# Kernel tuning notes

Measured on AMD Instinct MI355X. Metric: run time of the kernel, lower is better.

Reference implementation:

```python
import jax, jax.numpy as jnp
import numpy as np

N_NODES = 100000

def _gcn_conv(x, W, b, src, dst, ew, num_nodes):
    # x: [N, Fin], W: [Fin, Fout], src/dst: [Etot], ew: [Etot]
    xw = x @ W                                   # [N, Fout]
    deg = jax.ops.segment_sum(ew, dst, num_segments=num_nodes)   # [N]
    dinv = jnp.where(deg > 0, jax.lax.rsqrt(jnp.where(deg > 0, deg, 1.0)), 0.0)
    norm = dinv[src] * ew * dinv[dst]            # [Etot]
    msg = xw[src] * norm[:, None]                # [Etot, Fout] gather-transform
    out = jax.ops.segment_sum(msg, dst, num_segments=num_nodes)  # scatter-add
    return out + b

def setup_inputs() -> dict:
    key = jax.random.key(0)
    k1, k2, k3, k4, k5, k6, k7 = jax.random.split(key, 7)
    N, E, F_IN, HID, CLS = N_NODES, 1600000, 128, 64, 32
    x = jax.random.normal(k1, (N, F_IN), dtype=jnp.float32)
    edge_index = jax.random.randint(k2, (2, E), 0, N, dtype=jnp.int64)
    edge_weight = jax.random.uniform(k3, (E,), dtype=jnp.float32)
    s1 = 1.0 / np.sqrt(F_IN)
    s2 = 1.0 / np.sqrt(HID)
    W1 = jax.random.uniform(k4, (F_IN, HID), dtype=jnp.float32, minval=-s1, maxval=s1)
    b1 = jnp.zeros((HID,), dtype=jnp.float32)
    W2 = jax.random.uniform(k5, (HID, CLS), dtype=jnp.float32, minval=-s2, maxval=s2)
    b2 = jnp.zeros((CLS,), dtype=jnp.float32)
    return {"x": x, "edge_index": edge_index, "edge_weight": edge_weight,
            "W1": W1, "b1": b1, "W2": W2, "b2": b2}

def reference(x, edge_index, edge_weight, W1, b1, W2, b2):
    N = x.shape[0]
    # add self-loops with weight 1 (PyG GCNConv default)
    loop = jnp.arange(N, dtype=edge_index.dtype)
    src = jnp.concatenate([edge_index[0], loop])
    dst = jnp.concatenate([edge_index[1], loop])
    ew = jnp.concatenate([edge_weight, jnp.ones((N,), dtype=edge_weight.dtype)])
    h = _gcn_conv(x, W1, b1, src, dst, ew, N)
    h = jax.nn.relu(h)
    # dropout is identity in eval mode
    out = _gcn_conv(h, W2, b2, src, dst, ew, N)
    return out
```

## Files before the change

### kernel.cpp

```cpp
#include <hip/hip_runtime.h>

#define FIN 128
#define HID 64
#define CLS 32

#define BSH 7
#define BNODES 128
#define GB 256
#define BCAP 4096
#define SCAP 6272
#define NBUKP 800

using bfrag = __attribute__((ext_vector_type(8))) short;
using cfrag = __attribute__((ext_vector_type(4))) float;

__device__ inline unsigned short f2bf(float x) {
  unsigned u = __float_as_uint(x);
  return (unsigned short)((u + 0x7FFFu + ((u >> 16) & 1u)) >> 16);
}
__device__ inline void bf8_to_f32(int4 v, float* f) {
  f[0] = __uint_as_float((unsigned)v.x << 16);
  f[1] = __uint_as_float((unsigned)v.x & 0xFFFF0000u);
  f[2] = __uint_as_float((unsigned)v.y << 16);
  f[3] = __uint_as_float((unsigned)v.y & 0xFFFF0000u);
  f[4] = __uint_as_float((unsigned)v.z << 16);
  f[5] = __uint_as_float((unsigned)v.z & 0xFFFF0000u);
  f[6] = __uint_as_float((unsigned)v.w << 16);
  f[7] = __uint_as_float((unsigned)v.w & 0xFFFF0000u);
}

__global__ __launch_bounds__(1024) void k_sort_wpack(const int* __restrict__ src,
                                                     const int* __restrict__ dst,
                                                     const float* __restrict__ ew,
                                                     int2* __restrict__ recsA,
                                                     int* __restrict__ gcntT,
                                                     int* __restrict__ loffB,
                                                     const float* __restrict__ W1,
                                                     const float* __restrict__ W2,
                                                     unsigned short* __restrict__ wp1,
                                                     unsigned short* __restrict__ wp2,
                                                     int E, int CHUNK, int NBUK) {
  __shared__ int2 stage[SCAP];
  __shared__ int lcnt[NBUKP];
  __shared__ int loff[NBUKP];
  __shared__ int lcur[NBUKP];
  __shared__ int ssum[1024];
  const int b = blockIdx.x, t = threadIdx.x;

  if (b >= GB) {
    int t2 = (b - GB) * 1024 + t;
    for (int i = t2; i < 16 * 512; i += 2048) {
      int f = i >> 9, l = (i >> 3) & 63, j = i & 7;
      int ks = f >> 2, nt = f & 3;
      int k = ks * 32 + (l >> 4) * 8 + j;
      int n = nt * 16 + (l & 15);
      wp1[i] = f2bf(W1[k * 64 + n]);
    }
    for (int i = t2; i < 4 * 512; i += 2048) {
      int f = i >> 9, l = (i >> 3) & 63, j = i & 7;
      int ks = f >> 1, nt = f & 1;
      int k = ks * 32 + (l >> 4) * 8 + j;
      int n = nt * 16 + (l & 15);
      wp2[i] = f2bf(W2[k * 32 + n]);
    }
    return;
  }

  const int s = b * CHUNK, e = min(E, s + CHUNK);
  const int m = e - s;

  for (int i = t; i < NBUK; i += 1024) lcnt[i] = 0;
  __syncthreads();
  for (int p = s + t; p < e; p += 1024)
    atomicAdd(&lcnt[dst[p] >> BSH], 1);
  __syncthreads();

  int c = (t < NBUK) ? lcnt[t] : 0;
  ssum[t] = c;
  __syncthreads();
  for (int off = 1; off < 1024; off <<= 1) {
    int v = (t >= off) ? ssum[t - off] : 0;
    __syncthreads();
    ssum[t] += v;
    __syncthreads();
  }
  if (t < NBUK) { loff[t] = ssum[t] - c; lcur[t] = ssum[t] - c; }
  if (t == 0) loff[NBUK] = m;
  __syncthreads();

  for (int p = s + t; p < e; p += 1024) {
    int d = dst[p];
    int bk = d >> BSH;
    int pos = atomicAdd(&lcur[bk], 1);
    stage[pos] = make_int2(src[p] | ((d & (BNODES - 1)) << 17), __float_as_int(ew[p]));
  }
  __syncthreads();

  for (int p = t; p < m; p += 1024) recsA[s + p] = stage[p];
  for (int i = t; i < NBUK; i += 1024) gcntT[i * GB + b] = lcnt[i];
  for (int i = t; i <= NBUK; i += 1024) loffB[b * NBUKP + i] = loff[i];
}

__global__ __launch_bounds__(256) void k_scan_sums(const int* __restrict__ counts,
                                                   int* __restrict__ bsum, int N) {
  __shared__ int s[256];
  int base = blockIdx.x * 4096 + threadIdx.x * 16;
  int t = 0;
#pragma unroll
  for (int j = 0; j < 16; ++j)
    if (base + j < N) t += counts[base + j];
  s[threadIdx.x] = t;
  __syncthreads();
  for (int off = 128; off > 0; off >>= 1) {
    if (threadIdx.x < off) s[threadIdx.x] += s[threadIdx.x + off];
    __syncthreads();
  }
  if (threadIdx.x == 0) bsum[blockIdx.x] = s[0];
}

__global__ __launch_bounds__(256) void k_scan_emit(const int* __restrict__ counts,
                                                   const int* __restrict__ bsum,
                                                   int* __restrict__ rowstart, int N, int nb) {
  __shared__ int sb[256];
  __shared__ int s[256];
  const int t = threadIdx.x;
  int bv = (t < nb) ? bsum[t] : 0;
  sb[t] = bv;
  __syncthreads();
  for (int off = 1; off < 256; off <<= 1) {
    int u = (t >= off) ? sb[t - off] : 0;
    __syncthreads();
    sb[t] += u;
    __syncthreads();
  }
  sb[t] -= bv;
  __syncthreads();
  const int bbase = sb[blockIdx.x];

  int base = blockIdx.x * 4096 + t * 16;
  int c[16];
  int tsum = 0;
#pragma unroll
  for (int j = 0; j < 16; ++j) {
    c[j] = (base + j < N) ? counts[base + j] : 0;
    tsum += c[j];
  }
  s[t] = tsum;
  __syncthreads();
  for (int off = 1; off < 256; off <<= 1) {
    int v = (t >= off) ? s[t - off] : 0;
    __syncthreads();
    s[t] += v;
    __syncthreads();
  }
  int run = bbase + s[t] - tsum;
#pragma unroll
  for (int j = 0; j < 16; ++j) {
    if (base + j < N) rowstart[base + j] = run;
    run += c[j];
  }
}

__global__ __launch_bounds__(256) void k_bucket(const int2* __restrict__ recsA,
                                                const int* __restrict__ goff,
                                                const int* __restrict__ loffB,
                                                int2* __restrict__ pairs,
                                                float* __restrict__ dinv,
                                                int* __restrict__ rowstart,
                                                int N, int E, int CHUNK, int NBUK) {
  __shared__ int2 lrec[BCAP];
  __shared__ int2 sout[BCAP];
  __shared__ int cnt[BNODES];
  __shared__ int cur[BNODES];
  __shared__ int sbuf[BNODES];
  __shared__ float degs[BNODES];
  __shared__ float dl[BNODES];
  const int b = blockIdx.x;
  const int t = threadIdx.x;
  const int bstart = goff[b * GB];
  const int bend = (b + 1 < NBUK) ? goff[(b + 1) * GB] : E;
  int m = bend - bstart;
  if (m > BCAP) m = BCAP;

  if (t < BNODES) { cnt[t] = 0; degs[t] = 1.0f; }
  __syncthreads();

  {
    int ls = loffB[t * NBUKP + b];
    int le = loffB[t * NBUKP + b + 1];
    int doff = goff[b * GB + t] - bstart;
    const int2* sp = recsA + (size_t)t * CHUNK + ls;
    int len = le - ls;
    for (int j = 0; j < len; ++j) {
      if (doff + j < BCAP) lrec[doff + j] = sp[j];
    }
  }
  __syncthreads();

  for (int p = t; p < m; p += 256) {
    int2 r = lrec[p];
    int d = (r.x >> 17) & (BNODES - 1);
    atomicAdd(&cnt[d], 1);
    atomicAdd(&degs[d], __int_as_float(r.y));
  }
  __syncthreads();
  if (t < BNODES) sbuf[t] = cnt[t];
  __syncthreads();
  for (int off = 1; off < BNODES; off <<= 1) {
    int v = (t < BNODES && t >= off) ? sbuf[t - off] : 0;
    __syncthreads();
    if (t < BNODES) sbuf[t] += v;
    __syncthreads();
  }
  if (t < BNODES) {
    int ls = sbuf[t] - cnt[t];
    cur[t] = ls;
    float di = rsqrtf(degs[t]);
    dl[t] = di;
    int node = b * BNODES + t;
    if (node < N) { dinv[node] = di; rowstart[node] = bstart + ls; }
  }
  __syncthreads();
  for (int p = t; p < m; p += 256) {
    int2 r = lrec[p];
    int d = (r.x >> 17) & (BNODES - 1);
    int pos = atomicAdd(&cur[d], 1);
    float c = __int_as_float(r.y) * dl[d];
    sout[pos] = make_int2(r.x & 0x1FFFF, __float_as_int(c));
  }
  __syncthreads();
  for (int p = t; p < m; p += 256) pairs[bstart + p] = sout[p];
}

template <int K, int F, bool ABF16>
__global__ __launch_bounds__(256, 4) void mfma_gemm(const void* __restrict__ xv,
                                                    const unsigned short* __restrict__ wp,
                                                    const float* __restrict__ scale,
                                                    unsigned short* __restrict__ y, int N) {
  constexpr int KS = K / 32;
  constexpr int NT = F / 16;
  const int lane = threadIdx.x & 63;
  const int quad = lane >> 4;
  const int col = lane & 15;
  const int row0 = blockIdx.x * 64 + (threadIdx.x >> 6) * 16;
  if (row0 >= N) return;

  bfrag bf[KS * NT];
#pragma unroll
  for (int f = 0; f < KS * NT; ++f)
    bf[f] = *(const bfrag*)(wp + f * 512 + lane * 8);

  cfrag acc[NT] = {};

  int row_a = row0 + col;
  if (row_a >= N) row_a = N - 1;

#pragma unroll
  for (int ks = 0; ks < KS; ++ks) {
    bfrag af;
    if (ABF16) {
      const unsigned short* xp = (const unsigned short*)xv + (size_t)row_a * K + quad * 8;
      af = *(const bfrag*)(xp + ks * 32);
    } else {
      const float* xp = (const float*)xv + (size_t)row_a * K + quad * 8;
      float4 a0 = *(const float4*)(xp + ks * 32);
      float4 a1 = *(const float4*)(xp + ks * 32 + 4);
      af[0] = (short)f2bf(a0.x); af[1] = (short)f2bf(a0.y);
      af[2] = (short)f2bf(a0.z); af[3] = (short)f2bf(a0.w);
      af[4] = (short)f2bf(a1.x); af[5] = (short)f2bf(a1.y);
      af[6] = (short)f2bf(a1.z); af[7] = (short)f2bf(a1.w);
    }
#pragma unroll
    for (int nt = 0; nt < NT; ++nt)
      acc[nt] = __builtin_amdgcn_mfma_f32_16x16x32_bf16(af, bf[ks * NT + nt], acc[nt], 0, 0, 0);
  }

  float scr[4];
#pragma unroll
  for (int r = 0; r < 4; ++r) {
    int row = row0 + quad * 4 + r;
    scr[r] = (row < N) ? scale[row] : 0.f;
  }
#pragma unroll
  for (int nt = 0; nt < NT; ++nt)
#pragma unroll
    for (int r = 0; r < 4; ++r) {
      int row = row0 + quad * 4 + r;
      if (row < N)
        y[(size_t)row * F + nt * 16 + col] = f2bf(scr[r] * acc[nt][r]);
    }
}

template <int F, bool BF16OUT>
__global__ __launch_bounds__(256) void pull_agg(const unsigned short* __restrict__ xs,
                                                const int2* __restrict__ pairs,
                                                const int* __restrict__ rowstart,
                                                const float* __restrict__ dinv,
                                                const float* __restrict__ b,
                                                void* __restrict__ outv, int N, int E) {
  constexpr int LPN = F / 8;
  constexpr int NPB = 256 / LPN;
  const int g = blockIdx.x * NPB + threadIdx.x / LPN;
  const int f8 = (threadIdx.x % LPN) * 8;
  if (g >= N) return;

  const int start = rowstart[g];
  const int end = (g + 1 < N) ? rowstart[g + 1] : E;
  const float di = dinv[g];

  float acc[8];
  {
    int4 v = *(const int4*)&xs[(size_t)g * F + f8];
    float xf[8];
    bf8_to_f32(v, xf);
    float4 b0 = *(const float4*)&b[f8];
    float4 b1 = *(const float4*)&b[f8 + 4];
    acc[0] = fmaf(di, xf[0], b0.x); acc[1] = fmaf(di, xf[1], b0.y);
    acc[2] = fmaf(di, xf[2], b0.z); acc[3] = fmaf(di, xf[3], b0.w);
    acc[4] = fmaf(di, xf[4], b1.x); acc[5] = fmaf(di, xf[5], b1.y);
    acc[6] = fmaf(di, xf[6], b1.z); acc[7] = fmaf(di, xf[7], b1.w);
  }

  int p = start;
  for (; p + 2 <= end; p += 2) {
    int2 p0 = pairs[p];
    int2 p1 = pairs[p + 1];
    int4 v0 = *(const int4*)&xs[(size_t)p0.x * F + f8];
    int4 v1 = *(const int4*)&xs[(size_t)p1.x * F + f8];
    float c0 = __int_as_float(p0.y), c1 = __int_as_float(p1.y);
    float x0[8], x1[8];
    bf8_to_f32(v0, x0);
    bf8_to_f32(v1, x1);
#pragma unroll
    for (int j = 0; j < 8; ++j) acc[j] = fmaf(c0, x0[j], acc[j]);
#pragma unroll
    for (int j = 0; j < 8; ++j) acc[j] = fmaf(c1, x1[j], acc[j]);
  }
  if (p < end) {
    int2 pa = pairs[p];
    int4 va = *(const int4*)&xs[(size_t)pa.x * F + f8];
    float ca = __int_as_float(pa.y);
    float xa[8];
    bf8_to_f32(va, xa);
#pragma unroll
    for (int j = 0; j < 8; ++j) acc[j] = fmaf(ca, xa[j], acc[j]);
  }

  if (BF16OUT) {
    unsigned short* out = (unsigned short*)outv;
    ushort4 o0, o1;
    o0.x = f2bf(fmaxf(acc[0], 0.f)); o0.y = f2bf(fmaxf(acc[1], 0.f));
    o0.z = f2bf(fmaxf(acc[2], 0.f)); o0.w = f2bf(fmaxf(acc[3], 0.f));
    o1.x = f2bf(fmaxf(acc[4], 0.f)); o1.y = f2bf(fmaxf(acc[5], 0.f));
    o1.z = f2bf(fmaxf(acc[6], 0.f)); o1.w = f2bf(fmaxf(acc[7], 0.f));
    *(ushort4*)&out[(size_t)g * F + f8] = o0;
    *(ushort4*)&out[(size_t)g * F + f8 + 4] = o1;
  } else {
    float* out = (float*)outv;
    *(float4*)&out[(size_t)g * F + f8] = make_float4(acc[0], acc[1], acc[2], acc[3]);
    *(float4*)&out[(size_t)g * F + f8 + 4] = make_float4(acc[4], acc[5], acc[6], acc[7]);
  }
}

extern "C" void kernel_launch(void* const* d_in, const int* in_sizes, int n_in,
                              void* d_out, int out_size, void* d_ws, size_t ws_size,
                              hipStream_t stream) {
  const float* x  = (const float*)d_in[0];
  const int*   ei = (const int*)d_in[1];
  const float* ew = (const float*)d_in[2];
  const float* W1 = (const float*)d_in[3];
  const float* b1 = (const float*)d_in[4];
  const float* W2 = (const float*)d_in[5];
  const float* b2 = (const float*)d_in[6];
  float* out = (float*)d_out;

  const int N = in_sizes[0] / FIN;
  const int E = in_sizes[2];
  const int* src = ei;
  const int* dst = ei + E;

  const int NBUK = (N + BNODES - 1) >> BSH;
  const int M = NBUK * GB;
  const int CHUNK = (E + GB - 1) / GB;
  const int nbM = (M + 4095) / 4096;

  float* wsf      = (float*)d_ws;
  float* dinv     = wsf;
  int*   rowstart = (int*)(dinv + N);
  int*   gcntT    = rowstart + N;
  int*   loffB    = gcntT + M;
  int*   bsum     = loffB + GB * NBUKP;
  int2*  recsA    = (int2*)(bsum + 256);
  int2*  pairs    = recsA + E;
  unsigned short* xs1 = (unsigned short*)(pairs + E);
  unsigned short* out1b = xs1 + (size_t)N * HID;
  unsigned short* xs2 = xs1;
  unsigned short* wp1 = out1b + (size_t)N * HID;
  unsigned short* wp2 = wp1 + 16 * 512;

  k_sort_wpack<<<GB + 2, 1024, 0, stream>>>(src, dst, ew, recsA, gcntT, loffB,
                                            W1, W2, wp1, wp2, E, CHUNK, NBUK);
  k_scan_sums<<<nbM, 256, 0, stream>>>(gcntT, bsum, M);
  k_scan_emit<<<nbM, 256, 0, stream>>>(gcntT, bsum, gcntT, M, nbM);
  k_bucket<<<NBUK, 256, 0, stream>>>(recsA, gcntT, loffB, pairs, dinv, rowstart,
                                     N, E, CHUNK, NBUK);

  mfma_gemm<FIN, HID, false><<<(N + 63) / 64, 256, 0, stream>>>(x, wp1, dinv, xs1, N);
  pull_agg<HID, true><<<(N + 31) / 32, 256, 0, stream>>>(xs1, pairs, rowstart, dinv, b1, out1b, N, E);

  mfma_gemm<HID, CLS, true><<<(N + 63) / 64, 256, 0, stream>>>(out1b, wp2, dinv, xs2, N);
  pull_agg<CLS, false><<<(N + 63) / 64, 256, 0, stream>>>(xs2, pairs, rowstart, dinv, b2, out, N, E);
}
```

Measured before the change: 242.7 us.

## Replace global scan kernels with per-bucket local scan and atomic cursor allocation

Removes the two global prefix-scan kernels. Each bucket block now scans its own 256 per-chunk counts and claims an output range in the pairs array through an atomicAdd on a global cursor, which the weight-pack block resets to zero. Because buckets are no longer laid out contiguously in node order, an explicit rowend array is written and pull_agg reads it instead of rowstart[g+1]. This saves two kernel launches and a pass over the count matrix. In exchange, the pairs layout is no longer node-ordered, so gather locality across adjacent nodes in pull_agg may be somewhat worse.

```diff
diff --git a/kernel.cpp b/kernel.cpp
--- a/kernel.cpp
+++ b/kernel.cpp
@@ -39,6 +39,7 @@
                                                      const float* __restrict__ W2,
                                                      unsigned short* __restrict__ wp1,
                                                      unsigned short* __restrict__ wp2,
+                                                     int* __restrict__ cursor,
                                                      int E, int CHUNK, int NBUK) {
   __shared__ int2 stage[SCAP];
   __shared__ int lcnt[NBUKP];
@@ -48,15 +49,15 @@
   const int b = blockIdx.x, t = threadIdx.x;
 
   if (b >= GB) {
-    int t2 = (b - GB) * 1024 + t;
-    for (int i = t2; i < 16 * 512; i += 2048) {
+    if (t == 0) *cursor = 0;
+    for (int i = t; i < 16 * 512; i += 1024) {
       int f = i >> 9, l = (i >> 3) & 63, j = i & 7;
       int ks = f >> 2, nt = f & 3;
       int k = ks * 32 + (l >> 4) * 8 + j;
       int n = nt * 16 + (l & 15);
       wp1[i] = f2bf(W1[k * 64 + n]);
     }
-    for (int i = t2; i < 4 * 512; i += 2048) {
+    for (int i = t; i < 4 * 512; i += 1024) {
       int f = i >> 9, l = (i >> 3) & 63, j = i & 7;
       int ks = f >> 1, nt = f & 1;
       int k = ks * 32 + (l >> 4) * 8 + j;
@@ -101,98 +102,52 @@
   for (int i = t; i <= NBUK; i += 1024) loffB[b * NBUKP + i] = loff[i];
 }
 
-__global__ __launch_bounds__(256) void k_scan_sums(const int* __restrict__ counts,
-                                                   int* __restrict__ bsum, int N) {
-  __shared__ int s[256];
-  int base = blockIdx.x * 4096 + threadIdx.x * 16;
-  int t = 0;
-#pragma unroll
-  for (int j = 0; j < 16; ++j)
-    if (base + j < N) t += counts[base + j];
-  s[threadIdx.x] = t;
-  __syncthreads();
-  for (int off = 128; off > 0; off >>= 1) {
-    if (threadIdx.x < off) s[threadIdx.x] += s[threadIdx.x + off];
-    __syncthreads();
-  }
-  if (threadIdx.x == 0) bsum[blockIdx.x] = s[0];
-}
-
-__global__ __launch_bounds__(256) void k_scan_emit(const int* __restrict__ counts,
-                                                   const int* __restrict__ bsum,
-                                                   int* __restrict__ rowstart, int N, int nb) {
-  __shared__ int sb[256];
-  __shared__ int s[256];
-  const int t = threadIdx.x;
-  int bv = (t < nb) ? bsum[t] : 0;
-  sb[t] = bv;
-  __syncthreads();
-  for (int off = 1; off < 256; off <<= 1) {
-    int u = (t >= off) ? sb[t - off] : 0;
-    __syncthreads();
-    sb[t] += u;
-    __syncthreads();
-  }
-  sb[t] -= bv;
-  __syncthreads();
-  const int bbase = sb[blockIdx.x];
-
-  int base = blockIdx.x * 4096 + t * 16;
-  int c[16];
-  int tsum = 0;
-#pragma unroll
-  for (int j = 0; j < 16; ++j) {
-    c[j] = (base + j < N) ? counts[base + j] : 0;
-    tsum += c[j];
-  }
-  s[t] = tsum;
-  __syncthreads();
-  for (int off = 1; off < 256; off <<= 1) {
-    int v = (t >= off) ? s[t - off] : 0;
-    __syncthreads();
-    s[t] += v;
-    __syncthreads();
-  }
-  int run = bbase + s[t] - tsum;
-#pragma unroll
-  for (int j = 0; j < 16; ++j) {
-    if (base + j < N) rowstart[base + j] = run;
-    run += c[j];
-  }
-}
-
 __global__ __launch_bounds__(256) void k_bucket(const int2* __restrict__ recsA,
-                                                const int* __restrict__ goff,
+                                                const int* __restrict__ gcntT,
                                                 const int* __restrict__ loffB,
                                                 int2* __restrict__ pairs,
                                                 float* __restrict__ dinv,
                                                 int* __restrict__ rowstart,
+                                                int* __restrict__ rowend,
+                                                int* __restrict__ cursor,
                                                 int N, int E, int CHUNK, int NBUK) {
   __shared__ int2 lrec[BCAP];
   __shared__ int2 sout[BCAP];
+  __shared__ int boff[256];
   __shared__ int cnt[BNODES];
   __shared__ int cur[BNODES];
   __shared__ int sbuf[BNODES];
   __shared__ float degs[BNODES];
   __shared__ float dl[BNODES];
+  __shared__ int basesh;
   const int b = blockIdx.x;
   const int t = threadIdx.x;
-  const int bstart = goff[b * GB];
-  const int bend = (b + 1 < NBUK) ? goff[(b + 1) * GB] : E;
-  int m = bend - bstart;
+
+  int bc = gcntT[b * GB + t];
+  boff[t] = bc;
+  __syncthreads();
+  for (int off = 1; off < 256; off <<= 1) {
+    int v = (t >= off) ? boff[t - off] : 0;
+    __syncthreads();
+    boff[t] += v;
+    __syncthreads();
+  }
+  int myoff = boff[t] - bc;
+  int total = boff[255];
+  if (t == 0) basesh = atomicAdd(cursor, total);
+  if (t < BNODES) { cnt[t] = 0; degs[t] = 1.0f; }
+  __syncthreads();
+  const int bstart = basesh;
+  int m = total;
   if (m > BCAP) m = BCAP;
-
-  if (t < BNODES) { cnt[t] = 0; degs[t] = 1.0f; }
-  __syncthreads();
 
   {
     int ls = loffB[t * NBUKP + b];
     int le = loffB[t * NBUKP + b + 1];
-    int doff = goff[b * GB + t] - bstart;
     const int2* sp = recsA + (size_t)t * CHUNK + ls;
     int len = le - ls;
     for (int j = 0; j < len; ++j) {
-      if (doff + j < BCAP) lrec[doff + j] = sp[j];
+      if (myoff + j < BCAP) lrec[myoff + j] = sp[j];
     }
   }
   __syncthreads();
@@ -218,7 +173,11 @@
     float di = rsqrtf(degs[t]);
     dl[t] = di;
     int node = b * BNODES + t;
-    if (node < N) { dinv[node] = di; rowstart[node] = bstart + ls; }
+    if (node < N) {
+      dinv[node] = di;
+      rowstart[node] = bstart + ls;
+      rowend[node] = bstart + ls + cnt[t];
+    }
   }
   __syncthreads();
   for (int p = t; p < m; p += 256) {
@@ -295,9 +254,10 @@
 __global__ __launch_bounds__(256) void pull_agg(const unsigned short* __restrict__ xs,
                                                 const int2* __restrict__ pairs,
                                                 const int* __restrict__ rowstart,
+                                                const int* __restrict__ rowend,
                                                 const float* __restrict__ dinv,
                                                 const float* __restrict__ b,
-                                                void* __restrict__ outv, int N, int E) {
+                                                void* __restrict__ outv, int N) {
   constexpr int LPN = F / 8;
   constexpr int NPB = 256 / LPN;
   const int g = blockIdx.x * NPB + threadIdx.x / LPN;
@@ -305,7 +265,7 @@
   if (g >= N) return;
 
   const int start = rowstart[g];
-  const int end = (g + 1 < N) ? rowstart[g + 1] : E;
+  const int end = rowend[g];
   const float di = dinv[g];
 
   float acc[8];
@@ -382,15 +342,15 @@
   const int NBUK = (N + BNODES - 1) >> BSH;
   const int M = NBUK * GB;
   const int CHUNK = (E + GB - 1) / GB;
-  const int nbM = (M + 4095) / 4096;
 
   float* wsf      = (float*)d_ws;
   float* dinv     = wsf;
   int*   rowstart = (int*)(dinv + N);
-  int*   gcntT    = rowstart + N;
+  int*   rowend   = rowstart + N;
+  int*   gcntT    = rowend + N;
   int*   loffB    = gcntT + M;
-  int*   bsum     = loffB + GB * NBUKP;
-  int2*  recsA    = (int2*)(bsum + 256);
+  int*   cursor   = loffB + GB * NBUKP;
+  int2*  recsA    = (int2*)(cursor + 4);
   int2*  pairs    = recsA + E;
   unsigned short* xs1 = (unsigned short*)(pairs + E);
   unsigned short* out1b = xs1 + (size_t)N * HID;
@@ -398,16 +358,16 @@
   unsigned short* wp1 = out1b + (size_t)N * HID;
   unsigned short* wp2 = wp1 + 16 * 512;
 
-  k_sort_wpack<<<GB + 2, 1024, 0, stream>>>(src, dst, ew, recsA, gcntT, loffB,
-                                            W1, W2, wp1, wp2, E, CHUNK, NBUK);
-  k_scan_sums<<<nbM, 256, 0, stream>>>(gcntT, bsum, M);
-  k_scan_emit<<<nbM, 256, 0, stream>>>(gcntT, bsum, gcntT, M, nbM);
+  k_sort_wpack<<<GB + 1, 1024, 0, stream>>>(src, dst, ew, recsA, gcntT, loffB,
+                                            W1, W2, wp1, wp2, cursor, E, CHUNK, NBUK);
   k_bucket<<<NBUK, 256, 0, stream>>>(recsA, gcntT, loffB, pairs, dinv, rowstart,
-                                     N, E, CHUNK, NBUK);
+                                     rowend, cursor, N, E, CHUNK, NBUK);
 
   mfma_gemm<FIN, HID, false><<<(N + 63) / 64, 256, 0, stream>>>(x, wp1, dinv, xs1, N);
-  pull_agg<HID, true><<<(N + 31) / 32, 256, 0, stream>>>(xs1, pairs, rowstart, dinv, b1, out1b, N, E);
+  pull_agg<HID, true><<<(N + 31) / 32, 256, 0, stream>>>(xs1, pairs, rowstart, rowend,
+                                                         dinv, b1, out1b, N);
 
   mfma_gemm<HID, CLS, true><<<(N + 63) / 64, 256, 0, stream>>>(out1b, wp2, dinv, xs2, N);
-  pull_agg<CLS, false><<<(N + 63) / 64, 256, 0, stream>>>(xs2, pairs, rowstart, dinv, b2, out, N, E);
-}
+  pull_agg<CLS, false><<<(N + 63) / 64, 256, 0, stream>>>(xs2, pairs, rowstart, rowend,
+                                                          dinv, b2, out, N);
+}
```

Result: slower. 269.2 us (+10.9%).

## Fuse layer-1 GEMM into sort kernel and apply source dinv during aggregation

Applied to the files above, without the earlier changes.

The first X@W1 GEMM now runs as extra blocks of the edge-sort kernel, packing W1 from shared memory, so it can overlap with the sorting and one launch disappears. Because dinv is not known yet when the GEMM runs, the layer-1 aggregation multiplies each edge coefficient by dinv[src] with an extra gather per edge, and squares dinv for the self term. The trade is a second random dinv load per edge in layer 1 and 64KB of dynamic shared memory on the fused kernel, which can lower occupancy of the sort blocks.

```diff
diff --git a/kernel.cpp b/kernel.cpp
--- a/kernel.cpp
+++ b/kernel.cpp
@@ -10,6 +10,11 @@
 #define BCAP 4096
 #define SCAP 6272
 #define NBUKP 800
+
+#define SM_STAGE 0
+#define SM_LCNT  50176
+#define SM_SSUM  (50176 + 9600)
+#define SM_BYTES (50176 + 9600 + 4096)
 
 using bfrag = __attribute__((ext_vector_type(8))) short;
 using cfrag = __attribute__((ext_vector_type(4))) float;
@@ -29,34 +34,23 @@
   f[7] = __uint_as_float((unsigned)v.w & 0xFFFF0000u);
 }
 
-__global__ __launch_bounds__(1024) void k_sort_wpack(const int* __restrict__ src,
-                                                     const int* __restrict__ dst,
-                                                     const float* __restrict__ ew,
-                                                     int2* __restrict__ recsA,
-                                                     int* __restrict__ gcntT,
-                                                     int* __restrict__ loffB,
-                                                     const float* __restrict__ W1,
-                                                     const float* __restrict__ W2,
-                                                     unsigned short* __restrict__ wp1,
-                                                     unsigned short* __restrict__ wp2,
-                                                     int E, int CHUNK, int NBUK) {
-  __shared__ int2 stage[SCAP];
-  __shared__ int lcnt[NBUKP];
-  __shared__ int loff[NBUKP];
-  __shared__ int lcur[NBUKP];
-  __shared__ int ssum[1024];
+__global__ __launch_bounds__(1024) void k_sort_gemm(const int* __restrict__ src,
+                                                    const int* __restrict__ dst,
+                                                    const float* __restrict__ ew,
+                                                    int2* __restrict__ recsA,
+                                                    int* __restrict__ gcntT,
+                                                    int* __restrict__ loffB,
+                                                    const float* __restrict__ W1,
+                                                    const float* __restrict__ W2,
+                                                    unsigned short* __restrict__ wp2,
+                                                    const float* __restrict__ x,
+                                                    unsigned short* __restrict__ xs1,
+                                                    int E, int CHUNK, int NBUK, int N) {
+  extern __shared__ char sm[];
   const int b = blockIdx.x, t = threadIdx.x;
 
-  if (b >= GB) {
-    int t2 = (b - GB) * 1024 + t;
-    for (int i = t2; i < 16 * 512; i += 2048) {
-      int f = i >> 9, l = (i >> 3) & 63, j = i & 7;
-      int ks = f >> 2, nt = f & 3;
-      int k = ks * 32 + (l >> 4) * 8 + j;
-      int n = nt * 16 + (l & 15);
-      wp1[i] = f2bf(W1[k * 64 + n]);
-    }
-    for (int i = t2; i < 4 * 512; i += 2048) {
+  if (b == GB) {
+    for (int i = t; i < 4 * 512; i += 1024) {
       int f = i >> 9, l = (i >> 3) & 63, j = i & 7;
       int ks = f >> 1, nt = f & 1;
       int k = ks * 32 + (l >> 4) * 8 + j;
@@ -65,6 +59,63 @@
     }
     return;
   }
+
+  if (b > GB) {
+    float* w1s = (float*)sm;
+    for (int i = t; i < FIN * HID; i += 1024) w1s[i] = W1[i];
+    __syncthreads();
+    const int lane = t & 63;
+    const int quad = lane >> 4;
+    const int col = lane & 15;
+    const int row0 = (b - GB - 1) * 256 + (t >> 6) * 16;
+    if (row0 >= N) return;
+
+    bfrag bf[16];
+#pragma unroll
+    for (int ks = 0; ks < 4; ++ks)
+#pragma unroll
+      for (int nt = 0; nt < 4; ++nt) {
+        bfrag v;
+#pragma unroll
+        for (int j = 0; j < 8; ++j)
+          v[j] = (short)f2bf(w1s[(ks * 32 + quad * 8 + j) * HID + nt * 16 + col]);
+        bf[ks * 4 + nt] = v;
+      }
+
+    cfrag acc[4] = {};
+    int row_a = row0 + col;
+    if (row_a >= N) row_a = N - 1;
+    const float* xp = x + (size_t)row_a * FIN + quad * 8;
+
+#pragma unroll
+    for (int ks = 0; ks < 4; ++ks) {
+      float4 a0 = *(const float4*)(xp + ks * 32);
+      float4 a1 = *(const float4*)(xp + ks * 32 + 4);
+      bfrag af;
+      af[0] = (short)f2bf(a0.x); af[1] = (short)f2bf(a0.y);
+      af[2] = (short)f2bf(a0.z); af[3] = (short)f2bf(a0.w);
+      af[4] = (short)f2bf(a1.x); af[5] = (short)f2bf(a1.y);
+      af[6] = (short)f2bf(a1.z); af[7] = (short)f2bf(a1.w);
+#pragma unroll
+      for (int nt = 0; nt < 4; ++nt)
+        acc[nt] = __builtin_amdgcn_mfma_f32_16x16x32_bf16(af, bf[ks * 4 + nt], acc[nt], 0, 0, 0);
+    }
+#pragma unroll
+    for (int nt = 0; nt < 4; ++nt)
+#pragma unroll
+      for (int r = 0; r < 4; ++r) {
+        int row = row0 + quad * 4 + r;
+        if (row < N)
+          xs1[(size_t)row * HID + nt * 16 + col] = f2bf(acc[nt][r]);
+      }
+    return;
+  }
+
+  int2* stage = (int2*)(sm + SM_STAGE);
+  int* lcnt = (int*)(sm + SM_LCNT);
+  int* loff = lcnt + NBUKP;
+  int* lcur = loff + NBUKP;
+  int* ssum = (int*)(sm + SM_SSUM);
 
   const int s = b * CHUNK, e = min(E, s + CHUNK);
   const int m = e - s;
@@ -232,11 +283,11 @@
   for (int p = t; p < m; p += 256) pairs[bstart + p] = sout[p];
 }
 
-template <int K, int F, bool ABF16>
-__global__ __launch_bounds__(256, 4) void mfma_gemm(const void* __restrict__ xv,
-                                                    const unsigned short* __restrict__ wp,
-                                                    const float* __restrict__ scale,
-                                                    unsigned short* __restrict__ y, int N) {
+template <int K, int F>
+__global__ __launch_bounds__(256, 4) void mfma_gemm2(const unsigned short* __restrict__ xv,
+                                                     const unsigned short* __restrict__ wp,
+                                                     const float* __restrict__ scale,
+                                                     unsigned short* __restrict__ y, int N) {
   constexpr int KS = K / 32;
   constexpr int NT = F / 16;
   const int lane = threadIdx.x & 63;
@@ -251,25 +302,13 @@
     bf[f] = *(const bfrag*)(wp + f * 512 + lane * 8);
 
   cfrag acc[NT] = {};
-
   int row_a = row0 + col;
   if (row_a >= N) row_a = N - 1;
+  const unsigned short* xp = xv + (size_t)row_a * K + quad * 8;
 
 #pragma unroll
   for (int ks = 0; ks < KS; ++ks) {
-    bfrag af;
-    if (ABF16) {
-      const unsigned short* xp = (const unsigned short*)xv + (size_t)row_a * K + quad * 8;
-      af = *(const bfrag*)(xp + ks * 32);
-    } else {
-      const float* xp = (const float*)xv + (size_t)row_a * K + quad * 8;
-      float4 a0 = *(const float4*)(xp + ks * 32);
-      float4 a1 = *(const float4*)(xp + ks * 32 + 4);
-      af[0] = (short)f2bf(a0.x); af[1] = (short)f2bf(a0.y);
-      af[2] = (short)f2bf(a0.z); af[3] = (short)f2bf(a0.w);
-      af[4] = (short)f2bf(a1.x); af[5] = (short)f2bf(a1.y);
-      af[6] = (short)f2bf(a1.z); af[7] = (short)f2bf(a1.w);
-    }
+    bfrag af = *(const bfrag*)(xp + ks * 32);
 #pragma unroll
     for (int nt = 0; nt < NT; ++nt)
       acc[nt] = __builtin_amdgcn_mfma_f32_16x16x32_bf16(af, bf[ks * NT + nt], acc[nt], 0, 0, 0);
@@ -291,7 +330,7 @@
     }
 }
 
-template <int F, bool BF16OUT>
+template <int F, bool BF16OUT, bool DG>
 __global__ __launch_bounds__(256) void pull_agg(const unsigned short* __restrict__ xs,
                                                 const int2* __restrict__ pairs,
                                                 const int* __restrict__ rowstart,
@@ -307,6 +346,7 @@
   const int start = rowstart[g];
   const int end = (g + 1 < N) ? rowstart[g + 1] : E;
   const float di = dinv[g];
+  const float selfc = DG ? di * di : di;
 
   float acc[8];
   {
@@ -315,10 +355,10 @@
     bf8_to_f32(v, xf);
     float4 b0 = *(const float4*)&b[f8];
     float4 b1 = *(const float4*)&b[f8 + 4];
-    acc[0] = fmaf(di, xf[0], b0.x); acc[1] = fmaf(di, xf[1], b0.y);
-    acc[2] = fmaf(di, xf[2], b0.z); acc[3] = fmaf(di, xf[3], b0.w);
-    acc[4] = fmaf(di, xf[4], b1.x); acc[5] = fmaf(di, xf[5], b1.y);
-    acc[6] = fmaf(di, xf[6], b1.z); acc[7] = fmaf(di, xf[7], b1.w);
+    acc[0] = fmaf(selfc, xf[0], b0.x); acc[1] = fmaf(selfc, xf[1], b0.y);
+    acc[2] = fmaf(selfc, xf[2], b0.z); acc[3] = fmaf(selfc, xf[3], b0.w);
+    acc[4] = fmaf(selfc, xf[4], b1.x); acc[5] = fmaf(selfc, xf[5], b1.y);
+    acc[6] = fmaf(selfc, xf[6], b1.z); acc[7] = fmaf(selfc, xf[7], b1.w);
   }
 
   int p = start;
@@ -328,6 +368,7 @@
     int4 v0 = *(const int4*)&xs[(size_t)p0.x * F + f8];
     int4 v1 = *(const int4*)&xs[(size_t)p1.x * F + f8];
     float c0 = __int_as_float(p0.y), c1 = __int_as_float(p1.y);
+    if (DG) { c0 *= dinv[p0.x]; c1 *= dinv[p1.x]; }
     float x0[8], x1[8];
     bf8_to_f32(v0, x0);
     bf8_to_f32(v1, x1);
@@ -340,6 +381,7 @@
     int2 pa = pairs[p];
     int4 va = *(const int4*)&xs[(size_t)pa.x * F + f8];
     float ca = __int_as_float(pa.y);
+    if (DG) ca *= dinv[pa.x];
     float xa[8];
     bf8_to_f32(va, xa);
 #pragma unroll
@@ -383,6 +425,7 @@
   const int M = NBUK * GB;
   const int CHUNK = (E + GB - 1) / GB;
   const int nbM = (M + 4095) / 4096;
+  const int NG = (N + 255) / 256;
 
   float* wsf      = (float*)d_ws;
   float* dinv     = wsf;
@@ -395,19 +438,19 @@
   unsigned short* xs1 = (unsigned short*)(pairs + E);
   unsigned short* out1b = xs1 + (size_t)N * HID;
   unsigned short* xs2 = xs1;
-  unsigned short* wp1 = out1b + (size_t)N * HID;
-  unsigned short* wp2 = wp1 + 16 * 512;
-
-  k_sort_wpack<<<GB + 2, 1024, 0, stream>>>(src, dst, ew, recsA, gcntT, loffB,
-                                            W1, W2, wp1, wp2, E, CHUNK, NBUK);
+  unsigned short* wp2 = out1b + (size_t)N * HID;
+
+  k_sort_gemm<<<GB + 1 + NG, 1024, SM_BYTES, stream>>>(src, dst, ew, recsA, gcntT,
+                                                       loffB, W1, W2, wp2, x, xs1,
+                                                       E, CHUNK, NBUK, N);
   k_scan_sums<<<nbM, 256, 0, stream>>>(gcntT, bsum, M);
   k_scan_emit<<<nbM, 256, 0, stream>>>(gcntT, bsum, gcntT, M, nbM);
   k_bucket<<<NBUK, 256, 0, stream>>>(recsA, gcntT, loffB, pairs, dinv, rowstart,
                                      N, E, CHUNK, NBUK);
 
-  mfma_gemm<FIN, HID, false><<<(N + 63) / 64, 256, 0, stream>>>(x, wp1, dinv, xs1, N);
-  pull_agg<HID, true><<<(N + 31) / 32, 256, 0, stream>>>(xs1, pairs, rowstart, dinv, b1, out1b, N, E);
-
-  mfma_gemm<HID, CLS, true><<<(N + 63) / 64, 256, 0, stream>>>(out1b, wp2, dinv, xs2, N);
-  pull_agg<CLS, false><<<(N + 63) / 64, 256, 0, stream>>>(xs2, pairs, rowstart, dinv, b2, out, N, E);
-}
+  pull_agg<HID, true, true><<<(N + 31) / 32, 256, 0, stream>>>(xs1, pairs, rowstart,
+                                                               dinv, b1, out1b, N, E);
+  mfma_gemm2<HID, CLS><<<(N + 63) / 64, 256, 0, stream>>>(out1b, wp2, dinv, xs2, N);
+  pull_agg<CLS, false, false><<<(N + 63) / 64, 256, 0, stream>>>(xs2, pairs, rowstart,
+                                                                 dinv, b2, out, N, E);
+}
```

After: 239.9 us. Within noise of the previous version (-1.2%).
